# Performance work log

Hardware: AMD Instinct MI355X
Metric: run time of the kernel (lower is better)

The kernel has to match this reference:

```python
import jax, jax.numpy as jnp
import numpy as np

DIM = 1024
NUM_HEADS = 16
HEAD_DIM = DIM // NUM_HEADS
SCALE = HEAD_DIM ** -0.5


def setup_inputs() -> dict:
    key = jax.random.key(0)
    k1, k2, k3 = jax.random.split(key, 3)
    B, N = 4, 2048
    x = jax.random.normal(k1, (B, N, DIM), dtype=jnp.float32)
    W_qkv = jax.random.normal(k2, (DIM, 3 * DIM), dtype=jnp.float32) * (DIM ** -0.5)
    b_qkv = jnp.zeros((3 * DIM,), dtype=jnp.float32)
    W_proj = jax.random.normal(k3, (DIM, DIM), dtype=jnp.float32) * (DIM ** -0.5)
    b_proj = jnp.zeros((DIM,), dtype=jnp.float32)
    return {"x": x, "W_qkv": W_qkv, "b_qkv": b_qkv, "W_proj": W_proj, "b_proj": b_proj}


def reference(x, W_qkv, b_qkv, W_proj, b_proj):
    B, N, D = x.shape
    qkv = x @ W_qkv + b_qkv                       # [B, N, 3D]
    qkv = qkv.reshape(B, N, 3, NUM_HEADS, HEAD_DIM)
    qkv = jnp.transpose(qkv, (2, 0, 3, 1, 4))     # [3, B, H, N, hd]
    q, k, v = qkv[0], qkv[1], qkv[2]
    attn = jnp.einsum('bhnd,bhmd->bhnm', q, k) * SCALE
    attn = jax.nn.softmax(attn, axis=-1)
    out = jnp.einsum('bhnm,bhmd->bhnd', attn, v)  # [B, H, N, hd]
    out = jnp.transpose(out, (0, 2, 1, 3)).reshape(B, N, D)
    return out @ W_proj + b_proj
```

## Files before the change

kernel.cpp:

```cpp
#include <hip/hip_runtime.h>
#include <hip/hip_bf16.h>

#define BATCH 4
#define SEQ   2048
#define DIM   1024
#define NHEAD 16
#define HDIM  64
#define ROWS  (BATCH * SEQ)
#define LS    72
#define GLS   68
#define QSCALE 0.18033688011f

typedef __bf16 bf16x8 __attribute__((ext_vector_type(8)));
typedef float  f32x4  __attribute__((ext_vector_type(4)));
typedef float  f32x16 __attribute__((ext_vector_type(16)));

static __device__ __forceinline__ uint pack2(float a, float b) {
    ushort ua = __builtin_bit_cast(ushort, (__bf16)a);
    ushort ub = __builtin_bit_cast(ushort, (__bf16)b);
    return (uint)ua | ((uint)ub << 16);
}
#define PLSWAP(a, b) asm volatile("v_permlane32_swap_b32 %0, %1" : "+v"(a), "+v"(b))

__global__ __launch_bounds__(256)
void convert_bf16_kernel(const float* __restrict__ in, ushort* __restrict__ out, int n8) {
    int stride = gridDim.x * blockDim.x;
    for (int i = blockIdx.x * blockDim.x + threadIdx.x; i < n8; i += stride) {
        float4 a = ((const float4*)in)[2 * i];
        float4 b = ((const float4*)in)[2 * i + 1];
        ushort u[8];
        u[0] = __builtin_bit_cast(ushort, (__bf16)a.x);
        u[1] = __builtin_bit_cast(ushort, (__bf16)a.y);
        u[2] = __builtin_bit_cast(ushort, (__bf16)a.z);
        u[3] = __builtin_bit_cast(ushort, (__bf16)a.w);
        u[4] = __builtin_bit_cast(ushort, (__bf16)b.x);
        u[5] = __builtin_bit_cast(ushort, (__bf16)b.y);
        u[6] = __builtin_bit_cast(ushort, (__bf16)b.z);
        u[7] = __builtin_bit_cast(ushort, (__bf16)b.w);
        ((uint4*)out)[i] = *(uint4*)u;
    }
}

__global__ __launch_bounds__(256)
void transpose_bf16_kernel(const float* __restrict__ W, ushort* __restrict__ Wt,
                           int K, int N) {
    __shared__ float tile[32][33];
    const int tx = threadIdx.x, ty = threadIdx.y;
    const int n0 = blockIdx.x * 32, k0 = blockIdx.y * 32;
#pragma unroll
    for (int i = 0; i < 4; ++i)
        tile[ty + 8 * i][tx] = W[(long)(k0 + ty + 8 * i) * N + n0 + tx];
    __syncthreads();
#pragma unroll
    for (int i = 0; i < 4; ++i) {
        float v = tile[tx][ty + 8 * i];
        Wt[(long)(n0 + ty + 8 * i) * K + k0 + tx] = __builtin_bit_cast(ushort, (__bf16)v);
    }
}

__global__ __launch_bounds__(256)
void gemm_mfma_kernel(const ushort* __restrict__ A, const ushort* __restrict__ Bt,
                      const float* __restrict__ bias,
                      int M, int N, int K, int mode,
                      __hip_bfloat16* __restrict__ Qb,
                      __hip_bfloat16* __restrict__ Kb,
                      __hip_bfloat16* __restrict__ Vb,
                      float* __restrict__ Cout) {
    const int t  = threadIdx.x;
    const int w  = t >> 6;
    const int l  = t & 63;
    const int c  = l & 15;
    const int g  = l >> 4;
    const int wr = w >> 1, wc = w & 1;
    const int row0 = blockIdx.y * 128;
    const int col0 = blockIdx.x * 128;

    __shared__ ushort As[128][GLS];
    __shared__ ushort Bs[128][GLS];

    const int sr = t >> 3;
    const int sa = t & 7;

    f32x4 acc[4][4];
#pragma unroll
    for (int i = 0; i < 4; ++i)
#pragma unroll
        for (int j = 0; j < 4; ++j) acc[i][j] = (f32x4){0.f, 0.f, 0.f, 0.f};

    for (int k0 = 0; k0 < K; k0 += 64) {
        __syncthreads();
#pragma unroll
        for (int i = 0; i < 4; ++i) {
            int row = i * 32 + sr;
            uint4 a = *(const uint4*)(A + (size_t)(row0 + row) * K + k0 + 8 * sa);
            *(uint2*)&As[row][8 * sa]     = make_uint2(a.x, a.y);
            *(uint2*)&As[row][8 * sa + 4] = make_uint2(a.z, a.w);
            uint4 b = *(const uint4*)(Bt + (size_t)(col0 + row) * K + k0 + 8 * sa);
            *(uint2*)&Bs[row][8 * sa]     = make_uint2(b.x, b.y);
            *(uint2*)&Bs[row][8 * sa + 4] = make_uint2(b.z, b.w);
        }
        __syncthreads();

#pragma unroll
        for (int ks = 0; ks < 2; ++ks) {
            bf16x8 am[4], bn[4];
#pragma unroll
            for (int mt = 0; mt < 4; ++mt) {
                uint2 a0 = *(const uint2*)&As[wr * 64 + mt * 16 + c][ks * 32 + 8 * g];
                uint2 a1 = *(const uint2*)&As[wr * 64 + mt * 16 + c][ks * 32 + 8 * g + 4];
                am[mt] = __builtin_bit_cast(bf16x8, make_uint4(a0.x, a0.y, a1.x, a1.y));
            }
#pragma unroll
            for (int nt = 0; nt < 4; ++nt) {
                uint2 b0 = *(const uint2*)&Bs[wc * 64 + nt * 16 + c][ks * 32 + 8 * g];
                uint2 b1 = *(const uint2*)&Bs[wc * 64 + nt * 16 + c][ks * 32 + 8 * g + 4];
                bn[nt] = __builtin_bit_cast(bf16x8, make_uint4(b0.x, b0.y, b1.x, b1.y));
            }
#pragma unroll
            for (int mt = 0; mt < 4; ++mt)
#pragma unroll
                for (int nt = 0; nt < 4; ++nt)
                    acc[mt][nt] = __builtin_amdgcn_mfma_f32_16x16x32_bf16(
                        am[mt], bn[nt], acc[mt][nt], 0, 0, 0);
        }
    }

    float bv[4];
#pragma unroll
    for (int nt = 0; nt < 4; ++nt) bv[nt] = bias[col0 + wc * 64 + nt * 16 + c];

#pragma unroll
    for (int mt = 0; mt < 4; ++mt) {
#pragma unroll
        for (int r = 0; r < 4; ++r) {
            int grow = row0 + wr * 64 + mt * 16 + 4 * g + r;
#pragma unroll
            for (int nt = 0; nt < 4; ++nt) {
                int gcol = col0 + wc * 64 + nt * 16 + c;
                float v = acc[mt][nt][r] + bv[nt];
                if (mode == 0) {
                    int s = gcol >> 10;
                    int hc = gcol & 1023;
                    int h = hc >> 6, d = hc & 63;
                    int bi = grow >> 11, n = grow & 2047;
                    size_t off = ((size_t)(bi * NHEAD + h) * SEQ + n) * HDIM + d;
                    if (s == 0) v *= QSCALE;
                    __hip_bfloat16 hb = __float2bfloat16(v);
                    if (s == 0)      Qb[off] = hb;
                    else if (s == 1) Kb[off] = hb;
                    else             Vb[off] = hb;
                } else {
                    Cout[(size_t)grow * N + gcol] = v;
                }
            }
        }
    }
}

__global__ __launch_bounds__(512)
void attn_mfma2_kernel(const ushort* __restrict__ Qg,
                       const ushort* __restrict__ Kg,
                       const ushort* __restrict__ Vg,
                       ushort* __restrict__ O) {
    const int id  = blockIdx.x;
    const int bh  = (id & 7) * 8 + ((id >> 3) & 7);
    const int qt  = id >> 6;
    const int t   = threadIdx.x;
    const int w   = t >> 6, l = t & 63;
    const int lo5 = l & 31, hi = l >> 5;
    const size_t base = (size_t)bh * SEQ * HDIM;
    const int q0  = qt * 256 + w * 32;

    __shared__ ushort Ks[2][64 * LS];
    __shared__ ushort Vt[2][64 * LS];

    bf16x8 qf[4];
    {
        const ushort* qrow = Qg + base + (size_t)(q0 + lo5) * HDIM + 8 * hi;
#pragma unroll
        for (int db = 0; db < 4; ++db)
            qf[db] = __builtin_bit_cast(bf16x8, *(const uint4*)(qrow + 16 * db));
    }

    const bool isV = (t < 256);
    const int vkp = t & 31, vcg = (t >> 5) & 7;
    const int u   = t & 255;
    const int ksr = u & 63, kch = u >> 6;
    const ushort* gptr = isV
        ? (Vg + base + (size_t)(2 * vkp) * HDIM + 8 * vcg)
        : (Kg + base + (size_t)ksr * HDIM + 16 * kch);
    const int second = isV ? HDIM : 8;

    auto stage = [&](int buf, uint4 a, uint4 b) {
        if (isV) {
            const uint* pa = (const uint*)&a;
            const uint* pb = (const uint*)&b;
#pragma unroll
            for (int e = 0; e < 8; ++e) {
                uint sel = (e & 1) ? 0x07060302u : 0x05040100u;
                uint packed = __builtin_amdgcn_perm(pb[e >> 1], pa[e >> 1], sel);
                *(uint*)&Vt[buf][(8 * vcg + e) * LS + 2 * vkp] = packed;
            }
        } else {
            ushort* p = &Ks[buf][ksr * LS + 16 * kch];
            *(uint4*)(p)     = a;
            *(uint4*)(p + 8) = b;
        }
    };

    uint4 r0 = *(const uint4*)(gptr);
    uint4 r1 = *(const uint4*)(gptr + second);
    stage(0, r0, r1);
    {
        const size_t off = (size_t)64 * HDIM;
        r0 = *(const uint4*)(gptr + off);
        r1 = *(const uint4*)(gptr + off + second);
    }
    __syncthreads();

    f32x16 o0, o1;
#pragma unroll
    for (int r = 0; r < 16; ++r) { o0[r] = 0.f; o1[r] = 0.f; }
    float m0 = -1e30f, ll = 0.f;

    for (int kt = 0; kt < 32; ++kt) {
        const int cur = kt & 1;
        if (kt < 31) stage(cur ^ 1, r0, r1);
        if (kt < 30) {
            const size_t off = (size_t)(kt + 2) * 64 * HDIM;
            r0 = *(const uint4*)(gptr + off);
            r1 = *(const uint4*)(gptr + off + second);
        }

        f32x16 s[2];
        __builtin_amdgcn_s_setprio(1);
#pragma unroll
        for (int kb = 0; kb < 2; ++kb) {
            f32x16 acc;
#pragma unroll
            for (int r = 0; r < 16; ++r) acc[r] = 0.f;
#pragma unroll
            for (int db = 0; db < 4; ++db) {
                uint4 araw = *(const uint4*)&Ks[cur][(kb * 32 + lo5) * LS + 16 * db + 8 * hi];
                bf16x8 af = __builtin_bit_cast(bf16x8, araw);
                acc = __builtin_amdgcn_mfma_f32_32x32x16_bf16(af, qf[db], acc, 0, 0, 0);
            }
            s[kb] = acc;
        }
        __builtin_amdgcn_s_setprio(0);

        float c0 = s[0][0], c1 = s[0][1];
#pragma unroll
        for (int r = 2; r < 16; r += 2) {
            c0 = fmaxf(fmaxf(c0, s[0][r]), s[0][r + 1]);
            c1 = fmaxf(fmaxf(c1, s[1][r]), s[1][r + 1]);
        }
        c0 = fmaxf(fmaxf(c0, s[1][0]), s[1][1]);
        float pmax = fmaxf(c0, c1);
        pmax = fmaxf(pmax, __shfl_xor(pmax, 32, 64));

        if (!__all(pmax <= m0 + 8.f)) {
            float mn = fmaxf(m0, pmax);
            float corr = __builtin_amdgcn_exp2f(m0 - mn);
#pragma unroll
            for (int r = 0; r < 16; ++r) { o0[r] *= corr; o1[r] *= corr; }
            ll *= corr;
            m0 = mn;
        }
        float a0 = 0.f, a1 = 0.f, a2 = 0.f, a3 = 0.f;
#pragma unroll
        for (int r = 0; r < 16; r += 2) {
            float p0 = __builtin_amdgcn_exp2f(s[0][r]     - m0); s[0][r]     = p0; a0 += p0;
            float p1 = __builtin_amdgcn_exp2f(s[0][r + 1] - m0); s[0][r + 1] = p1; a1 += p1;
            float p2 = __builtin_amdgcn_exp2f(s[1][r]     - m0); s[1][r]     = p2; a2 += p2;
            float p3 = __builtin_amdgcn_exp2f(s[1][r + 1] - m0); s[1][r + 1] = p3; a3 += p3;
        }
        float rs = (a0 + a1) + (a2 + a3);
        rs += __shfl_xor(rs, 32, 64);
        ll += rs;

        bf16x8 pbf[4];
#pragma unroll
        for (int kb = 0; kb < 2; ++kb)
#pragma unroll
            for (int kk = 0; kk < 2; ++kk) {
                const int b0 = kk * 8;
                uint w0 = pack2(s[kb][b0 + 0], s[kb][b0 + 1]);
                uint w1 = pack2(s[kb][b0 + 2], s[kb][b0 + 3]);
                uint w2 = pack2(s[kb][b0 + 4], s[kb][b0 + 5]);
                uint w3 = pack2(s[kb][b0 + 6], s[kb][b0 + 7]);
                PLSWAP(w0, w2);
                PLSWAP(w1, w3);
                pbf[kb * 2 + kk] = __builtin_bit_cast(bf16x8, make_uint4(w0, w1, w2, w3));
            }

        __builtin_amdgcn_s_setprio(1);
#pragma unroll
        for (int kb = 0; kb < 2; ++kb)
#pragma unroll
            for (int kk = 0; kk < 2; ++kk) {
                const int kcol = kb * 32 + kk * 16 + 8 * hi;
                uint4 vraw0 = *(const uint4*)&Vt[cur][lo5 * LS + kcol];
                bf16x8 vf0 = __builtin_bit_cast(bf16x8, vraw0);
                o0 = __builtin_amdgcn_mfma_f32_32x32x16_bf16(vf0, pbf[kb * 2 + kk], o0, 0, 0, 0);
                uint4 vraw1 = *(const uint4*)&Vt[cur][(lo5 + 32) * LS + kcol];
                bf16x8 vf1 = __builtin_bit_cast(bf16x8, vraw1);
                o1 = __builtin_amdgcn_mfma_f32_32x32x16_bf16(vf1, pbf[kb * 2 + kk], o1, 0, 0, 0);
            }
        __builtin_amdgcn_s_setprio(0);

        __syncthreads();
    }

    const float inv = 1.f / ll;
    const int b = bh >> 4, h = bh & 15;
    ushort* orow = O + (size_t)(b * SEQ + q0 + lo5) * DIM + h * HDIM;
#pragma unroll
    for (int j = 0; j < 4; ++j) {
        uint2 st;
        st.x = pack2(o0[4 * j + 0] * inv, o0[4 * j + 1] * inv);
        st.y = pack2(o0[4 * j + 2] * inv, o0[4 * j + 3] * inv);
        *(uint2*)(orow + 8 * j + 4 * hi) = st;
        st.x = pack2(o1[4 * j + 0] * inv, o1[4 * j + 1] * inv);
        st.y = pack2(o1[4 * j + 2] * inv, o1[4 * j + 3] * inv);
        *(uint2*)(orow + 32 + 8 * j + 4 * hi) = st;
    }
}

extern "C" void kernel_launch(void* const* d_in, const int* in_sizes, int n_in,
                              void* d_out, int out_size, void* d_ws, size_t ws_size,
                              hipStream_t stream) {
    const float* x      = (const float*)d_in[0];
    const float* W_qkv  = (const float*)d_in[1];
    const float* b_qkv  = (const float*)d_in[2];
    const float* W_proj = (const float*)d_in[3];
    const float* b_proj = (const float*)d_in[4];
    float* out = (float*)d_out;

    const size_t qkv_elems = (size_t)BATCH * NHEAD * SEQ * HDIM;
    char* ws = (char*)d_ws;
    ushort* xb      = (ushort*)ws;
    ushort* Wqkv_t  = (ushort*)(ws + qkv_elems * 2);
    ushort* Wproj_t = (ushort*)(ws + qkv_elems * 2 + (size_t)DIM * 3 * DIM * 2);
    char*   ws2     = ws + qkv_elems * 2 + (size_t)DIM * 3 * DIM * 2 + (size_t)DIM * DIM * 2;
    __hip_bfloat16* Qb = (__hip_bfloat16*)ws2;
    __hip_bfloat16* Kb = (__hip_bfloat16*)(ws2 + qkv_elems * 2);
    __hip_bfloat16* Vb = (__hip_bfloat16*)(ws2 + qkv_elems * 4);
    ushort* attnout = xb;

    convert_bf16_kernel<<<2048, 256, 0, stream>>>(x, xb, ROWS * DIM / 8);
    transpose_bf16_kernel<<<dim3(3 * DIM / 32, DIM / 32), dim3(32, 8), 0, stream>>>(
        W_qkv, Wqkv_t, DIM, 3 * DIM);
    transpose_bf16_kernel<<<dim3(DIM / 32, DIM / 32), dim3(32, 8), 0, stream>>>(
        W_proj, Wproj_t, DIM, DIM);

    gemm_mfma_kernel<<<dim3(3 * DIM / 128, ROWS / 128), 256, 0, stream>>>(
        xb, Wqkv_t, b_qkv, ROWS, 3 * DIM, DIM, 0, Qb, Kb, Vb, nullptr);

    attn_mfma2_kernel<<<dim3(512), 512, 0, stream>>>(
        (const ushort*)Qb, (const ushort*)Kb, (const ushort*)Vb, attnout);

    gemm_mfma_kernel<<<dim3(DIM / 128, ROWS / 128), 256, 0, stream>>>(
        attnout, Wproj_t, b_proj, ROWS, DIM, DIM, 1, nullptr, nullptr, nullptr, out);
}
```

Before: 223.1 us.

## Process two K/V tiles per barrier window and interleave QK with PV

The attention loop now stages two 64-key tiles per double-buffered window, so it runs 16 iterations with one barrier each instead of 32. Within a window, the QK of the second tile is issued before the PV of the first tile, so MFMA work can overlap the softmax dependency chain. This doubles LDS use per block and raises register pressure from extra prefetch registers and a second packed-P set. It also adds a launch-bounds hint of 4 waves-per-EU minimum, which may force spills.

```diff
diff --git a/kernel.cpp b/kernel.cpp
--- a/kernel.cpp
+++ b/kernel.cpp
@@ -10,6 +10,7 @@
 #define LS    72
 #define GLS   68
 #define QSCALE 0.18033688011f
+#define TILE  (64 * HDIM)
 
 typedef __bf16 bf16x8 __attribute__((ext_vector_type(8)));
 typedef float  f32x4  __attribute__((ext_vector_type(4)));
@@ -157,7 +158,7 @@
     }
 }
 
-__global__ __launch_bounds__(512)
+__global__ __launch_bounds__(512, 4)
 void attn_mfma2_kernel(const ushort* __restrict__ Qg,
                        const ushort* __restrict__ Kg,
                        const ushort* __restrict__ Vg,
@@ -171,8 +172,8 @@
     const size_t base = (size_t)bh * SEQ * HDIM;
     const int q0  = qt * 256 + w * 32;
 
-    __shared__ ushort Ks[2][64 * LS];
-    __shared__ ushort Vt[2][64 * LS];
+    __shared__ ushort Ks[2][2][64 * LS];
+    __shared__ ushort Vt[2][2][64 * LS];
 
     bf16x8 qf[4];
     {
@@ -191,7 +192,7 @@
         : (Kg + base + (size_t)ksr * HDIM + 16 * kch);
     const int second = isV ? HDIM : 8;
 
-    auto stage = [&](int buf, uint4 a, uint4 b) {
+    auto stage = [&](int buf, int tile, uint4 a, uint4 b) {
         if (isV) {
             const uint* pa = (const uint*)&a;
             const uint* pb = (const uint*)&b;
@@ -199,22 +200,27 @@
             for (int e = 0; e < 8; ++e) {
                 uint sel = (e & 1) ? 0x07060302u : 0x05040100u;
                 uint packed = __builtin_amdgcn_perm(pb[e >> 1], pa[e >> 1], sel);
-                *(uint*)&Vt[buf][(8 * vcg + e) * LS + 2 * vkp] = packed;
+                *(uint*)&Vt[buf][tile][(8 * vcg + e) * LS + 2 * vkp] = packed;
             }
         } else {
-            ushort* p = &Ks[buf][ksr * LS + 16 * kch];
+            ushort* p = &Ks[buf][tile][ksr * LS + 16 * kch];
             *(uint4*)(p)     = a;
             *(uint4*)(p + 8) = b;
         }
     };
 
-    uint4 r0 = *(const uint4*)(gptr);
-    uint4 r1 = *(const uint4*)(gptr + second);
-    stage(0, r0, r1);
+    uint4 ra0, ra1, rb0, rb1;
+    ra0 = *(const uint4*)(gptr);
+    ra1 = *(const uint4*)(gptr + second);
+    rb0 = *(const uint4*)(gptr + TILE);
+    rb1 = *(const uint4*)(gptr + TILE + second);
+    stage(0, 0, ra0, ra1);
+    stage(0, 1, rb0, rb1);
     {
-        const size_t off = (size_t)64 * HDIM;
-        r0 = *(const uint4*)(gptr + off);
-        r1 = *(const uint4*)(gptr + off + second);
+        ra0 = *(const uint4*)(gptr + 2 * TILE);
+        ra1 = *(const uint4*)(gptr + 2 * TILE + second);
+        rb0 = *(const uint4*)(gptr + 3 * TILE);
+        rb1 = *(const uint4*)(gptr + 3 * TILE + second);
     }
     __syncthreads();
 
@@ -223,91 +229,105 @@
     for (int r = 0; r < 16; ++r) { o0[r] = 0.f; o1[r] = 0.f; }
     float m0 = -1e30f, ll = 0.f;
 
-    for (int kt = 0; kt < 32; ++kt) {
-        const int cur = kt & 1;
-        if (kt < 31) stage(cur ^ 1, r0, r1);
-        if (kt < 30) {
-            const size_t off = (size_t)(kt + 2) * 64 * HDIM;
-            r0 = *(const uint4*)(gptr + off);
-            r1 = *(const uint4*)(gptr + off + second);
-        }
+    for (int win = 0; win < 16; ++win) {
+        const int cur = win & 1;
+        if (win < 15) {
+            stage(cur ^ 1, 0, ra0, ra1);
+            stage(cur ^ 1, 1, rb0, rb1);
+        }
+        if (win < 14) {
+            const size_t offA = (size_t)(2 * win + 4) * TILE;
+            ra0 = *(const uint4*)(gptr + offA);
+            ra1 = *(const uint4*)(gptr + offA + second);
+            rb0 = *(const uint4*)(gptr + offA + TILE);
+            rb1 = *(const uint4*)(gptr + offA + TILE + second);
+        }
+
+        auto qk = [&](int tile, f32x16* sout) {
+            __builtin_amdgcn_s_setprio(1);
+#pragma unroll
+            for (int kb = 0; kb < 2; ++kb) {
+                f32x16 acc;
+#pragma unroll
+                for (int r = 0; r < 16; ++r) acc[r] = 0.f;
+#pragma unroll
+                for (int db = 0; db < 4; ++db) {
+                    uint4 araw = *(const uint4*)&Ks[cur][tile][(kb * 32 + lo5) * LS + 16 * db + 8 * hi];
+                    bf16x8 af = __builtin_bit_cast(bf16x8, araw);
+                    acc = __builtin_amdgcn_mfma_f32_32x32x16_bf16(af, qf[db], acc, 0, 0, 0);
+                }
+                sout[kb] = acc;
+            }
+            __builtin_amdgcn_s_setprio(0);
+        };
+        auto softmax_pack = [&](f32x16* s, bf16x8* pbf) {
+            float c0 = s[0][0], c1 = s[0][1];
+#pragma unroll
+            for (int r = 2; r < 16; r += 2) {
+                c0 = fmaxf(fmaxf(c0, s[0][r]), s[0][r + 1]);
+                c1 = fmaxf(fmaxf(c1, s[1][r]), s[1][r + 1]);
+            }
+            c0 = fmaxf(fmaxf(c0, s[1][0]), s[1][1]);
+            float pmax = fmaxf(c0, c1);
+            pmax = fmaxf(pmax, __shfl_xor(pmax, 32, 64));
+            if (!__all(pmax <= m0 + 8.f)) {
+                float mn = fmaxf(m0, pmax);
+                float corr = __builtin_amdgcn_exp2f(m0 - mn);
+#pragma unroll
+                for (int r = 0; r < 16; ++r) { o0[r] *= corr; o1[r] *= corr; }
+                ll *= corr;
+                m0 = mn;
+            }
+            float a0 = 0.f, a1 = 0.f, a2 = 0.f, a3 = 0.f;
+#pragma unroll
+            for (int r = 0; r < 16; r += 2) {
+                float p0 = __builtin_amdgcn_exp2f(s[0][r]     - m0); s[0][r]     = p0; a0 += p0;
+                float p1 = __builtin_amdgcn_exp2f(s[0][r + 1] - m0); s[0][r + 1] = p1; a1 += p1;
+                float p2 = __builtin_amdgcn_exp2f(s[1][r]     - m0); s[1][r]     = p2; a2 += p2;
+                float p3 = __builtin_amdgcn_exp2f(s[1][r + 1] - m0); s[1][r + 1] = p3; a3 += p3;
+            }
+            float rs = (a0 + a1) + (a2 + a3);
+            rs += __shfl_xor(rs, 32, 64);
+            ll += rs;
+#pragma unroll
+            for (int kb = 0; kb < 2; ++kb)
+#pragma unroll
+                for (int kk = 0; kk < 2; ++kk) {
+                    const int b0 = kk * 8;
+                    uint w0 = pack2(s[kb][b0 + 0], s[kb][b0 + 1]);
+                    uint w1 = pack2(s[kb][b0 + 2], s[kb][b0 + 3]);
+                    uint w2 = pack2(s[kb][b0 + 4], s[kb][b0 + 5]);
+                    uint w3 = pack2(s[kb][b0 + 6], s[kb][b0 + 7]);
+                    PLSWAP(w0, w2);
+                    PLSWAP(w1, w3);
+                    pbf[kb * 2 + kk] = __builtin_bit_cast(bf16x8, make_uint4(w0, w1, w2, w3));
+                }
+        };
+        auto pv = [&](int tile, const bf16x8* pbf) {
+            __builtin_amdgcn_s_setprio(1);
+#pragma unroll
+            for (int kb = 0; kb < 2; ++kb)
+#pragma unroll
+                for (int kk = 0; kk < 2; ++kk) {
+                    const int kcol = kb * 32 + kk * 16 + 8 * hi;
+                    uint4 vraw0 = *(const uint4*)&Vt[cur][tile][lo5 * LS + kcol];
+                    bf16x8 vf0 = __builtin_bit_cast(bf16x8, vraw0);
+                    o0 = __builtin_amdgcn_mfma_f32_32x32x16_bf16(vf0, pbf[kb * 2 + kk], o0, 0, 0, 0);
+                    uint4 vraw1 = *(const uint4*)&Vt[cur][tile][(lo5 + 32) * LS + kcol];
+                    bf16x8 vf1 = __builtin_bit_cast(bf16x8, vraw1);
+                    o1 = __builtin_amdgcn_mfma_f32_32x32x16_bf16(vf1, pbf[kb * 2 + kk], o1, 0, 0, 0);
+                }
+            __builtin_amdgcn_s_setprio(0);
+        };
 
         f32x16 s[2];
-        __builtin_amdgcn_s_setprio(1);
-#pragma unroll
-        for (int kb = 0; kb < 2; ++kb) {
-            f32x16 acc;
-#pragma unroll
-            for (int r = 0; r < 16; ++r) acc[r] = 0.f;
-#pragma unroll
-            for (int db = 0; db < 4; ++db) {
-                uint4 araw = *(const uint4*)&Ks[cur][(kb * 32 + lo5) * LS + 16 * db + 8 * hi];
-                bf16x8 af = __builtin_bit_cast(bf16x8, araw);
-                acc = __builtin_amdgcn_mfma_f32_32x32x16_bf16(af, qf[db], acc, 0, 0, 0);
-            }
-            s[kb] = acc;
-        }
-        __builtin_amdgcn_s_setprio(0);
-
-        float c0 = s[0][0], c1 = s[0][1];
-#pragma unroll
-        for (int r = 2; r < 16; r += 2) {
-            c0 = fmaxf(fmaxf(c0, s[0][r]), s[0][r + 1]);
-            c1 = fmaxf(fmaxf(c1, s[1][r]), s[1][r + 1]);
-        }
-        c0 = fmaxf(fmaxf(c0, s[1][0]), s[1][1]);
-        float pmax = fmaxf(c0, c1);
-        pmax = fmaxf(pmax, __shfl_xor(pmax, 32, 64));
-
-        if (!__all(pmax <= m0 + 8.f)) {
-            float mn = fmaxf(m0, pmax);
-            float corr = __builtin_amdgcn_exp2f(m0 - mn);
-#pragma unroll
-            for (int r = 0; r < 16; ++r) { o0[r] *= corr; o1[r] *= corr; }
-            ll *= corr;
-            m0 = mn;
-        }
-        float a0 = 0.f, a1 = 0.f, a2 = 0.f, a3 = 0.f;
-#pragma unroll
-        for (int r = 0; r < 16; r += 2) {
-            float p0 = __builtin_amdgcn_exp2f(s[0][r]     - m0); s[0][r]     = p0; a0 += p0;
-            float p1 = __builtin_amdgcn_exp2f(s[0][r + 1] - m0); s[0][r + 1] = p1; a1 += p1;
-            float p2 = __builtin_amdgcn_exp2f(s[1][r]     - m0); s[1][r]     = p2; a2 += p2;
-            float p3 = __builtin_amdgcn_exp2f(s[1][r + 1] - m0); s[1][r + 1] = p3; a3 += p3;
-        }
-        float rs = (a0 + a1) + (a2 + a3);
-        rs += __shfl_xor(rs, 32, 64);
-        ll += rs;
-
-        bf16x8 pbf[4];
-#pragma unroll
-        for (int kb = 0; kb < 2; ++kb)
-#pragma unroll
-            for (int kk = 0; kk < 2; ++kk) {
-                const int b0 = kk * 8;
-                uint w0 = pack2(s[kb][b0 + 0], s[kb][b0 + 1]);
-                uint w1 = pack2(s[kb][b0 + 2], s[kb][b0 + 3]);
-                uint w2 = pack2(s[kb][b0 + 4], s[kb][b0 + 5]);
-                uint w3 = pack2(s[kb][b0 + 6], s[kb][b0 + 7]);
-                PLSWAP(w0, w2);
-                PLSWAP(w1, w3);
-                pbf[kb * 2 + kk] = __builtin_bit_cast(bf16x8, make_uint4(w0, w1, w2, w3));
-            }
-
-        __builtin_amdgcn_s_setprio(1);
-#pragma unroll
-        for (int kb = 0; kb < 2; ++kb)
-#pragma unroll
-            for (int kk = 0; kk < 2; ++kk) {
-                const int kcol = kb * 32 + kk * 16 + 8 * hi;
-                uint4 vraw0 = *(const uint4*)&Vt[cur][lo5 * LS + kcol];
-                bf16x8 vf0 = __builtin_bit_cast(bf16x8, vraw0);
-                o0 = __builtin_amdgcn_mfma_f32_32x32x16_bf16(vf0, pbf[kb * 2 + kk], o0, 0, 0, 0);
-                uint4 vraw1 = *(const uint4*)&Vt[cur][(lo5 + 32) * LS + kcol];
-                bf16x8 vf1 = __builtin_bit_cast(bf16x8, vraw1);
-                o1 = __builtin_amdgcn_mfma_f32_32x32x16_bf16(vf1, pbf[kb * 2 + kk], o1, 0, 0, 0);
-            }
-        __builtin_amdgcn_s_setprio(0);
+        bf16x8 pbf1[4], pbf2[4];
+        qk(0, s);
+        softmax_pack(s, pbf1);
+        qk(1, s);
+        pv(0, pbf1);
+        softmax_pack(s, pbf2);
+        pv(1, pbf2);
 
         __syncthreads();
     }
```

New measurement: 227.8 us. 2.1% more time.
